# Optimization experiments

Hardware: AMD Instinct MI355X
Metric: run time of the kernel (lower is better)

Reference implementation:

```python
import jax, jax.numpy as jnp
import numpy as np

Bsz, L, D, N = 2, 2048, 1024, 16
LN_EPS = 1e-5


def setup_inputs() -> dict:
    key = jax.random.key(0)
    ks = jax.random.split(key, 5)
    # A_log initialized as in the module: -log(arange(1, N+1)) broadcast over D
    A_log = -jnp.broadcast_to(jnp.log(jnp.arange(1, N + 1, dtype=jnp.float32))[None, :], (D, N))
    return {
        "x": jax.random.normal(ks[0], (Bsz, L, D), jnp.float32),
        "W_dt": jax.random.normal(ks[1], (D, D), jnp.float32) * 0.02,
        "b_dt": jnp.zeros((D,), jnp.float32),
        "W_B": jax.random.normal(ks[2], (N, D), jnp.float32) * 0.02,
        "W_C": jax.random.normal(ks[3], (N, D), jnp.float32) * 0.02,
        "D_param": jnp.ones((D,), jnp.float32),
        "A_log": A_log,
        "gamma": jnp.ones((D,), jnp.float32),
        "beta": jnp.zeros((D,), jnp.float32),
    }


def reference(x, W_dt, b_dt, W_B, W_C, D_param, A_log, gamma, beta):
    residual = x
    # LayerNorm (biased variance, eps=1e-5)
    mu = jnp.mean(x, axis=-1, keepdims=True)
    var = jnp.var(x, axis=-1, keepdims=True)
    xn = (x - mu) * jax.lax.rsqrt(var + LN_EPS) * gamma + beta

    dt = jax.nn.softplus(xn @ W_dt.T + b_dt)          # (B, L, D)
    A = -jnp.exp(A_log)                                # (D, N)
    B_in = xn @ W_B.T                                  # (B, L, N)
    C_in = xn @ W_C.T                                  # (B, L, N)

    A_bar = jnp.exp(dt[..., None] * A)                 # (B, L, D, N)
    # B_bar[t] * x[t] fused: dt * B_in * xn -> (B, L, D, N)
    Bx = dt[..., None] * B_in[:, :, None, :] * xn[..., None]

    def step(h, inputs):
        a_t, bx_t, c_t = inputs                        # (B,D,N), (B,D,N), (B,N)
        h = a_t * h + bx_t                             # (B, D, N)
        y_t = jnp.einsum('bn,bdn->bd', c_t, h)         # (B, D)
        return h, y_t

    h0 = jnp.zeros((x.shape[0], D, N), x.dtype)
    _, ys = jax.lax.scan(
        step, h0,
        (jnp.transpose(A_bar, (1, 0, 2, 3)),
         jnp.transpose(Bx, (1, 0, 2, 3)),
         jnp.transpose(C_in, (1, 0, 2))))
    y = jnp.transpose(ys, (1, 0, 2)) + D_param * residual
    return y
```

## Files before the change

kernel.cpp:

```cpp
#include <hip/hip_runtime.h>
#include <hip/hip_cooperative_groups.h>
#include <cstddef>

namespace cg = cooperative_groups;

#define Bsz 2
#define Lr  2048
#define Dr  1024
#define Nr  16
#define M_ROWS (Bsz*Lr)
#define NPAD   1088
#define CHUNK  32
#define NCH    (Lr/CHUNK)

#define BM 64
#define BN 64
#define BK 64
#define NK (Dr/BK)

typedef __attribute__((ext_vector_type(8))) __bf16 bf16x8;
typedef __attribute__((ext_vector_type(4))) float floatx4;

__device__ __forceinline__ unsigned short f2bf(float f) {
    unsigned u = __float_as_uint(f);
    u += 0x7fffu + ((u >> 16) & 1u);
    return (unsigned short)(u >> 16);
}

__device__ __forceinline__ float bf2f(unsigned short u) {
    return __uint_as_float(((unsigned)u) << 16);
}

__device__ __forceinline__ float softplus_f(float x) {
    if (x > 0.f) return x + __logf(1.f + __expf(-x));
    return __logf(1.f + __expf(x));
}

__device__ __forceinline__ void gload_lds16(const unsigned short* g, unsigned short* l) {
    __builtin_amdgcn_global_load_lds((const __attribute__((address_space(1))) void*)g,
                                     (__attribute__((address_space(3))) void*)l, 16, 0, 0);
}

__global__ __launch_bounds__(256) void ln_pack_kernel(const float* __restrict__ x,
                                                      const float* __restrict__ gamma,
                                                      const float* __restrict__ beta,
                                                      unsigned short* __restrict__ xnb,
                                                      const float* __restrict__ Wdt,
                                                      const float* __restrict__ WB,
                                                      const float* __restrict__ WC,
                                                      unsigned short* __restrict__ Wcat) {
    if (blockIdx.x >= M_ROWS) {
        int i = (blockIdx.x - M_ROWS) * 256 + threadIdx.x;
        int row = i >> 10;
        int col = i & 1023;
        float v;
        if (row < Dr)                 v = Wdt[i];
        else if (row < Dr + Nr)       v = WB[(row - Dr) * Dr + col];
        else if (row < Dr + 2*Nr)     v = WC[(row - Dr - Nr) * Dr + col];
        else                          v = 0.f;
        Wcat[i] = f2bf(v);
        return;
    }
    int row = blockIdx.x;
    int tid = threadIdx.x;
    const float4* xr = (const float4*)(x + (size_t)row * Dr);
    float4 v = xr[tid];
    float s  = v.x + v.y + v.z + v.w;
    float ss = v.x*v.x + v.y*v.y + v.z*v.z + v.w*v.w;
    #pragma unroll
    for (int off = 32; off > 0; off >>= 1) {
        s  += __shfl_down(s, off);
        ss += __shfl_down(ss, off);
    }
    __shared__ float red[8];
    int wid = tid >> 6;
    if ((tid & 63) == 0) { red[wid*2] = s; red[wid*2+1] = ss; }
    __syncthreads();
    if (tid == 0) {
        float S = 0.f, SS = 0.f;
        #pragma unroll
        for (int w = 0; w < 4; w++) { S += red[w*2]; SS += red[w*2+1]; }
        float mu  = S * (1.f/Dr);
        float var = SS * (1.f/Dr) - mu*mu;
        red[0] = mu;
        red[1] = rsqrtf(var + 1e-5f);
    }
    __syncthreads();
    float mu = red[0], rs = red[1];
    float4 g = ((const float4*)gamma)[tid], bt = ((const float4*)beta)[tid];
    float4 o;
    o.x = (v.x - mu) * rs * g.x + bt.x;
    o.y = (v.y - mu) * rs * g.y + bt.y;
    o.z = (v.z - mu) * rs * g.z + bt.z;
    o.w = (v.w - mu) * rs * g.w + bt.w;
    ushort4 ob;
    ob.x = f2bf(o.x); ob.y = f2bf(o.y); ob.z = f2bf(o.z); ob.w = f2bf(o.w);
    ((ushort4*)(xnb + (size_t)row * Dr))[tid] = ob;
}

__global__ __launch_bounds__(256) void gemm_kernel(const unsigned short* __restrict__ xnb,
                                                   const unsigned short* __restrict__ w,
                                                   const float* __restrict__ b_dt,
                                                   unsigned short* __restrict__ dt,
                                                   float* __restrict__ bin,
                                                   float* __restrict__ cin) {
    __shared__ unsigned short As[BM * BK];
    __shared__ unsigned short Bs[BN * BK];
    int tid  = threadIdx.x;
    int wave = tid >> 6;
    int lane = tid & 63;
    int lm   = lane & 15;
    int quad = lane >> 4;
    int bid  = blockIdx.x;
    int xcd  = bid & 7;
    int j0   = bid >> 3;
    int nt   = j0 % 17;
    int mt   = (j0 / 17) * 8 + xcd;
    int Mb = mt * BM;
    int Nb = nt * BN;
    int wm = (wave >> 1) * 32;
    int wn = (wave & 1)  * 32;
    int koff = (mt + nt) & (NK - 1);

    int r0 = tid >> 3,        cg0 = (tid & 7) ^ (r0 & 7);
    int r1 = (tid + 256) >> 3, cg1 = ((tid + 256) & 7) ^ (r1 & 7);
    const unsigned short* Ag0 = xnb + (size_t)(Mb + r0) * Dr + cg0 * 8;
    const unsigned short* Ag1 = xnb + (size_t)(Mb + r1) * Dr + cg1 * 8;
    const unsigned short* Bg0 = w   + (size_t)(Nb + r0) * Dr + cg0 * 8;
    const unsigned short* Bg1 = w   + (size_t)(Nb + r1) * Dr + cg1 * 8;
    unsigned short* Al0 = &As[(size_t)tid * 8];
    unsigned short* Al1 = &As[(size_t)(tid + 256) * 8];
    unsigned short* Bl0 = &Bs[(size_t)tid * 8];
    unsigned short* Bl1 = &Bs[(size_t)(tid + 256) * 8];

    floatx4 acc[2][2] = {};

    for (int kk = 0; kk < NK; kk++) {
        int k0 = ((kk + koff) & (NK - 1)) * BK;
        gload_lds16(Ag0 + k0, Al0);
        gload_lds16(Ag1 + k0, Al1);
        gload_lds16(Bg0 + k0, Bl0);
        gload_lds16(Bg1 + k0, Bl1);
        __syncthreads();
        #pragma unroll
        for (int s = 0; s < 2; s++) {
            int ra0 = wm + lm, ra1 = wm + 16 + lm;
            int rb0 = wn + lm, rb1 = wn + 16 + lm;
            int cg = s * 4 + quad;
            bf16x8 a0 = *(const bf16x8*)&As[ra0 * BK + ((cg ^ (ra0 & 7)) * 8)];
            bf16x8 a1 = *(const bf16x8*)&As[ra1 * BK + ((cg ^ (ra1 & 7)) * 8)];
            bf16x8 b0 = *(const bf16x8*)&Bs[rb0 * BK + ((cg ^ (rb0 & 7)) * 8)];
            bf16x8 b1 = *(const bf16x8*)&Bs[rb1 * BK + ((cg ^ (rb1 & 7)) * 8)];
            acc[0][0] = __builtin_amdgcn_mfma_f32_16x16x32_bf16(a0, b0, acc[0][0], 0, 0, 0);
            acc[0][1] = __builtin_amdgcn_mfma_f32_16x16x32_bf16(a0, b1, acc[0][1], 0, 0, 0);
            acc[1][0] = __builtin_amdgcn_mfma_f32_16x16x32_bf16(a1, b0, acc[1][0], 0, 0, 0);
            acc[1][1] = __builtin_amdgcn_mfma_f32_16x16x32_bf16(a1, b1, acc[1][1], 0, 0, 0);
        }
        __syncthreads();
    }

    #pragma unroll
    for (int i = 0; i < 2; i++) {
        int grow0 = Mb + wm + i * 16 + quad * 4;
        #pragma unroll
        for (int jj = 0; jj < 2; jj++) {
            int gcol = Nb + wn + jj * 16 + lm;
            #pragma unroll
            for (int r = 0; r < 4; r++) {
                float v = acc[i][jj][r];
                int row = grow0 + r;
                if (gcol < Dr) {
                    dt[(size_t)row * Dr + gcol] = f2bf(softplus_f(v + b_dt[gcol]));
                } else if (gcol < Dr + Nr) {
                    bin[(size_t)row * Nr + (gcol - Dr)] = v;
                } else if (gcol < Dr + 2*Nr) {
                    cin[(size_t)row * Nr + (gcol - Dr - Nr)] = v;
                }
            }
        }
    }
}

__global__ __launch_bounds__(256, 2) void scan_fused_kernel(
        const unsigned short* __restrict__ dtb,
        const unsigned short* __restrict__ xnb,
        const float* __restrict__ bin,
        const float* __restrict__ cin,
        const float* __restrict__ A_log,
        const float* __restrict__ x,
        const float* __restrict__ Dp,
        float* __restrict__ Pws,
        float* __restrict__ hendws,
        float* __restrict__ hinws,
        float* __restrict__ out) {
    cg::grid_group grid = cg::this_grid();
    int tid  = threadIdx.x;
    int bid  = blockIdx.x;
    int dblk = bid & 3;
    int ch   = (bid >> 2) & 63;
    int b    = bid >> 8;
    int d    = dblk * 256 + tid;
    size_t rowbase = (size_t)b * Lr + ch * CHUNK;

    float ac[16];
    #pragma unroll
    for (int i = 0; i < 4; i++) {
        float4 t = ((const float4*)(A_log + (size_t)d * Nr))[i];
        ac[i*4+0] = -__expf(t.x);
        ac[i*4+1] = -__expf(t.y);
        ac[i*4+2] = -__expf(t.z);
        ac[i*4+3] = -__expf(t.w);
    }

    __shared__ float lb[CHUNK * Nr];
    __shared__ float lc[CHUNK * Nr];
    for (int i = tid; i < CHUNK * Nr; i += 256) {
        lb[i] = bin[rowbase * Nr + i];
        lc[i] = cin[rowbase * Nr + i];
    }
    __syncthreads();

    float dtv[CHUNK], xv[CHUNK];
    {
        const unsigned short* dtp = dtb + rowbase * Dr + d;
        const unsigned short* xp  = xnb + rowbase * Dr + d;
        #pragma unroll
        for (int t = 0; t < CHUNK; t++) {
            dtv[t] = bf2f(dtp[(size_t)t * Dr]);
            xv[t]  = bf2f(xp[(size_t)t * Dr]);
        }
    }

    float h[16];
    #pragma unroll
    for (int n = 0; n < 16; n++) h[n] = 0.f;
    float S = 0.f;
    #pragma unroll
    for (int t = 0; t < CHUNK; t++) {
        float dv = dtv[t];
        S += dv;
        float cm = dv * xv[t];
        const float4* br4 = (const float4*)(lb + t * Nr);
        float4 q0 = br4[0], q1 = br4[1], q2 = br4[2], q3 = br4[3];
        float bb[16] = {q0.x,q0.y,q0.z,q0.w, q1.x,q1.y,q1.z,q1.w,
                        q2.x,q2.y,q2.z,q2.w, q3.x,q3.y,q3.z,q3.w};
        #pragma unroll
        for (int n = 0; n < 16; n++)
            h[n] = __expf(dv * ac[n]) * h[n] + cm * bb[n];
    }
    size_t obase = ((size_t)(b * NCH + ch) * Nr) * Dr + d;
    #pragma unroll
    for (int n = 0; n < 16; n++) {
        Pws[obase + (size_t)n * Dr]    = __expf(S * ac[n]);
        hendws[obase + (size_t)n * Dr] = h[n];
    }

    grid.sync();

    if (bid < 128) {
        int id = bid * 256 + tid;
        int b2 = id >> 14;
        int dn = id & 16383;
        size_t base = ((size_t)b2 * NCH) * (Nr * Dr) + dn;
        float hin = 0.f;
        for (int cb = 0; cb < NCH; cb += 4) {
            float p[4], he[4];
            #pragma unroll
            for (int u = 0; u < 4; u++) {
                size_t idx = base + (size_t)(cb + u) * (Nr * Dr);
                p[u]  = Pws[idx];
                he[u] = hendws[idx];
            }
            #pragma unroll
            for (int u = 0; u < 4; u++) {
                size_t idx = base + (size_t)(cb + u) * (Nr * Dr);
                hinws[idx] = hin;
                hin = p[u] * hin + he[u];
            }
        }
    }

    grid.sync();

    #pragma unroll
    for (int n = 0; n < 16; n++) h[n] = hinws[obase + (size_t)n * Dr];
    float dp = Dp[d];
    const float* xr = x   + rowbase * Dr + d;
    float* op       = out + rowbase * Dr + d;

    for (int tb = 0; tb < CHUNK; tb += 4) {
        float xr4[4];
        #pragma unroll
        for (int u = 0; u < 4; u++) xr4[u] = xr[(size_t)(tb + u) * Dr];
        #pragma unroll
        for (int u = 0; u < 4; u++) {
            int t = tb + u;
            float dv = dtv[t];
            float cm = dv * xv[t];
            const float4* br4 = (const float4*)(lb + t * Nr);
            const float4* cr4 = (const float4*)(lc + t * Nr);
            float4 q0 = br4[0], q1 = br4[1], q2 = br4[2], q3 = br4[3];
            float4 r0 = cr4[0], r1 = cr4[1], r2 = cr4[2], r3 = cr4[3];
            float bb[16] = {q0.x,q0.y,q0.z,q0.w, q1.x,q1.y,q1.z,q1.w,
                            q2.x,q2.y,q2.z,q2.w, q3.x,q3.y,q3.z,q3.w};
            float cc[16] = {r0.x,r0.y,r0.z,r0.w, r1.x,r1.y,r1.z,r1.w,
                            r2.x,r2.y,r2.z,r2.w, r3.x,r3.y,r3.z,r3.w};
            float y = 0.f;
            #pragma unroll
            for (int n = 0; n < 16; n++) {
                h[n] = __expf(dv * ac[n]) * h[n] + cm * bb[n];
                y += cc[n] * h[n];
            }
            op[(size_t)t * Dr] = y + dp * xr4[u];
        }
    }
}

__global__ __launch_bounds__(256) void scan1_kernel(const unsigned short* __restrict__ dtb,
                                                    const unsigned short* __restrict__ xnb,
                                                    const float* __restrict__ bin,
                                                    const float* __restrict__ A_log,
                                                    float* __restrict__ Pws,
                                                    float* __restrict__ hendws) {
    int d  = blockIdx.x * 256 + threadIdx.x;
    int ch = blockIdx.y;
    int b  = blockIdx.z;
    size_t rowbase = (size_t)b * Lr + ch * CHUNK;

    float ac[16];
    #pragma unroll
    for (int i = 0; i < 4; i++) {
        float4 t = ((const float4*)(A_log + (size_t)d * Nr))[i];
        ac[i*4+0] = -__expf(t.x);
        ac[i*4+1] = -__expf(t.y);
        ac[i*4+2] = -__expf(t.z);
        ac[i*4+3] = -__expf(t.w);
    }

    __shared__ float lb[CHUNK * Nr];
    for (int i = threadIdx.x; i < CHUNK * Nr; i += 256)
        lb[i] = bin[rowbase * Nr + i];
    __syncthreads();

    float h[16];
    #pragma unroll
    for (int n = 0; n < 16; n++) h[n] = 0.f;
    float S = 0.f;

    const unsigned short* dtp = dtb + rowbase * Dr + d;
    const unsigned short* xp  = xnb + rowbase * Dr + d;

    for (int tb = 0; tb < CHUNK; tb += 4) {
        float dt4[4], xv4[4];
        #pragma unroll
        for (int u = 0; u < 4; u++) {
            dt4[u] = bf2f(dtp[(size_t)(tb + u) * Dr]);
            xv4[u] = bf2f(xp[(size_t)(tb + u) * Dr]);
        }
        #pragma unroll
        for (int u = 0; u < 4; u++) {
            float dv = dt4[u];
            S += dv;
            float cm = dv * xv4[u];
            const float4* br4 = (const float4*)(lb + (tb + u) * Nr);
            float4 q0 = br4[0], q1 = br4[1], q2 = br4[2], q3 = br4[3];
            float bb[16] = {q0.x,q0.y,q0.z,q0.w, q1.x,q1.y,q1.z,q1.w,
                            q2.x,q2.y,q2.z,q2.w, q3.x,q3.y,q3.z,q3.w};
            #pragma unroll
            for (int n = 0; n < 16; n++)
                h[n] = __expf(dv * ac[n]) * h[n] + cm * bb[n];
        }
    }

    size_t obase = ((size_t)(b * NCH + ch) * Nr) * Dr + d;
    #pragma unroll
    for (int n = 0; n < 16; n++) {
        Pws[obase + (size_t)n * Dr]    = __expf(S * ac[n]);
        hendws[obase + (size_t)n * Dr] = h[n];
    }
}

__global__ __launch_bounds__(256) void combine_kernel(const float* __restrict__ Pws,
                                                      const float* __restrict__ hendws,
                                                      float* __restrict__ hinws) {
    int id = blockIdx.x * 256 + threadIdx.x;
    int b  = id >> 14;
    int dn = id & 16383;
    size_t base = ((size_t)b * NCH) * (Nr * Dr) + dn;
    float hin = 0.f;
    for (int cb = 0; cb < NCH; cb += 4) {
        float p[4], he[4];
        #pragma unroll
        for (int u = 0; u < 4; u++) {
            size_t idx = base + (size_t)(cb + u) * (Nr * Dr);
            p[u]  = Pws[idx];
            he[u] = hendws[idx];
        }
        #pragma unroll
        for (int u = 0; u < 4; u++) {
            size_t idx = base + (size_t)(cb + u) * (Nr * Dr);
            hinws[idx] = hin;
            hin = p[u] * hin + he[u];
        }
    }
}

__global__ __launch_bounds__(256) void scan2_kernel(const unsigned short* __restrict__ dtb,
                                                    const unsigned short* __restrict__ xnb,
                                                    const float* __restrict__ bin,
                                                    const float* __restrict__ cin,
                                                    const float* __restrict__ A_log,
                                                    const float* __restrict__ hinws,
                                                    const float* __restrict__ x,
                                                    const float* __restrict__ Dp,
                                                    float* __restrict__ out) {
    int d  = blockIdx.x * 256 + threadIdx.x;
    int ch = blockIdx.y;
    int b  = blockIdx.z;
    size_t rowbase = (size_t)b * Lr + ch * CHUNK;

    float ac[16];
    #pragma unroll
    for (int i = 0; i < 4; i++) {
        float4 t = ((const float4*)(A_log + (size_t)d * Nr))[i];
        ac[i*4+0] = -__expf(t.x);
        ac[i*4+1] = -__expf(t.y);
        ac[i*4+2] = -__expf(t.z);
        ac[i*4+3] = -__expf(t.w);
    }

    __shared__ float lb[CHUNK * Nr];
    __shared__ float lc[CHUNK * Nr];
    for (int i = threadIdx.x; i < CHUNK * Nr; i += 256) {
        lb[i] = bin[rowbase * Nr + i];
        lc[i] = cin[rowbase * Nr + i];
    }
    __syncthreads();

    size_t obase = ((size_t)(b * NCH + ch) * Nr) * Dr + d;
    float h[16];
    #pragma unroll
    for (int n = 0; n < 16; n++) h[n] = hinws[obase + (size_t)n * Dr];

    float dp = Dp[d];
    const unsigned short* dtp = dtb + rowbase * Dr + d;
    const unsigned short* xp  = xnb + rowbase * Dr + d;
    const float* xr           = x   + rowbase * Dr + d;
    float* op                 = out + rowbase * Dr + d;

    for (int tb = 0; tb < CHUNK; tb += 4) {
        float dt4[4], xv4[4], xr4[4];
        #pragma unroll
        for (int u = 0; u < 4; u++) {
            dt4[u] = bf2f(dtp[(size_t)(tb + u) * Dr]);
            xv4[u] = bf2f(xp[(size_t)(tb + u) * Dr]);
            xr4[u] = xr[(size_t)(tb + u) * Dr];
        }
        #pragma unroll
        for (int u = 0; u < 4; u++) {
            float dv = dt4[u];
            float cm = dv * xv4[u];
            const float4* br4 = (const float4*)(lb + (tb + u) * Nr);
            const float4* cr4 = (const float4*)(lc + (tb + u) * Nr);
            float4 q0 = br4[0], q1 = br4[1], q2 = br4[2], q3 = br4[3];
            float4 r0 = cr4[0], r1 = cr4[1], r2 = cr4[2], r3 = cr4[3];
            float bb[16] = {q0.x,q0.y,q0.z,q0.w, q1.x,q1.y,q1.z,q1.w,
                            q2.x,q2.y,q2.z,q2.w, q3.x,q3.y,q3.z,q3.w};
            float cc[16] = {r0.x,r0.y,r0.z,r0.w, r1.x,r1.y,r1.z,r1.w,
                            r2.x,r2.y,r2.z,r2.w, r3.x,r3.y,r3.z,r3.w};
            float y = 0.f;
            #pragma unroll
            for (int n = 0; n < 16; n++) {
                h[n] = __expf(dv * ac[n]) * h[n] + cm * bb[n];
                y += cc[n] * h[n];
            }
            op[(size_t)(tb + u) * Dr] = y + dp * xr4[u];
        }
    }
}

extern "C" void kernel_launch(void* const* d_in, const int* in_sizes, int n_in,
                              void* d_out, int out_size, void* d_ws, size_t ws_size,
                              hipStream_t stream) {
    const float* x      = (const float*)d_in[0];
    const float* W_dt   = (const float*)d_in[1];
    const float* b_dt   = (const float*)d_in[2];
    const float* W_B    = (const float*)d_in[3];
    const float* W_C    = (const float*)d_in[4];
    const float* Dparam = (const float*)d_in[5];
    const float* A_log  = (const float*)d_in[6];
    const float* gamma  = (const float*)d_in[7];
    const float* beta   = (const float*)d_in[8];
    float* out = (float*)d_out;

    char* ws = (char*)d_ws;
    unsigned short* xnb  = (unsigned short*)(ws);
    unsigned short* wcat = (unsigned short*)(ws + 8388608);
    unsigned short* dtb  = (unsigned short*)(ws + 10616832);
    float*          bin  = (float*)(ws + 19005440);
    float*          cin  = (float*)(ws + 19267584);
    float*          Pws  = (float*)(ws + 19529728);
    float*          hend = (float*)(ws + 27918336);
    float*          hin  = (float*)(ws + 36306944);

    ln_pack_kernel<<<M_ROWS + (NPAD * Dr) / 256, 256, 0, stream>>>(
        x, gamma, beta, xnb, W_dt, W_B, W_C, wcat);
    gemm_kernel<<<(M_ROWS / BM) * (NPAD / BN), 256, 0, stream>>>(xnb, wcat, b_dt, dtb, bin, cin);

    int maxBlk = 0;
    hipError_t qerr = hipOccupancyMaxActiveBlocksPerMultiprocessor(
        &maxBlk, (const void*)scan_fused_kernel, 256, 0);
    bool coop_done = false;
    if (qerr == hipSuccess && maxBlk >= 2) {
        void* args[] = {
            (void*)&dtb, (void*)&xnb, (void*)&bin, (void*)&cin, (void*)&A_log,
            (void*)&x, (void*)&Dparam, (void*)&Pws, (void*)&hend, (void*)&hin, (void*)&out
        };
        hipError_t e = hipLaunchCooperativeKernel((const void*)scan_fused_kernel,
                                                  dim3(512), dim3(256),
                                                  args, 0, stream);
        coop_done = (e == hipSuccess);
    }
    if (!coop_done) {
        dim3 sgrid(Dr / 256, NCH, Bsz);
        scan1_kernel<<<sgrid, 256, 0, stream>>>(dtb, xnb, bin, A_log, Pws, hend);
        combine_kernel<<<(Bsz * Dr * Nr) / 256, 256, 0, stream>>>(Pws, hend, hin);
        scan2_kernel<<<sgrid, 256, 0, stream>>>(dtb, xnb, bin, cin, A_log, hin, x, Dparam, out);
    }
}
```

Before: 159.6 us.

## Replace cooperative fused scan with three-kernel chunked scan using bf16 carries

Drops the cooperative-launch fused scan, whose two grid-wide barriers required it to fit in 512 resident blocks, and goes back to separate scan1/combine/scan2 kernels. The chunk length is halved to 16 so the launch has more blocks and each thread has a shorter serial recurrence. Chunk decay products, chunk-end states and carried-in states are stored as bf16 to cut workspace traffic. In exchange there are twice as many chunks for the serial combine pass and bf16 rounding on the carried states, which may cost accuracy.

```diff
diff --git a/kernel.cpp b/kernel.cpp
--- a/kernel.cpp
+++ b/kernel.cpp
@@ -1,8 +1,5 @@
 #include <hip/hip_runtime.h>
-#include <hip/hip_cooperative_groups.h>
 #include <cstddef>
-
-namespace cg = cooperative_groups;
 
 #define Bsz 2
 #define Lr  2048
@@ -10,7 +7,7 @@
 #define Nr  16
 #define M_ROWS (Bsz*Lr)
 #define NPAD   1088
-#define CHUNK  32
+#define CHUNK  16
 #define NCH    (Lr/CHUNK)
 
 #define BM 64
@@ -122,7 +119,7 @@
     int wn = (wave & 1)  * 32;
     int koff = (mt + nt) & (NK - 1);
 
-    int r0 = tid >> 3,        cg0 = (tid & 7) ^ (r0 & 7);
+    int r0 = tid >> 3,         cg0 = (tid & 7) ^ (r0 & 7);
     int r1 = (tid + 256) >> 3, cg1 = ((tid + 256) & 7) ^ (r1 & 7);
     const unsigned short* Ag0 = xnb + (size_t)(Mb + r0) * Dr + cg0 * 8;
     const unsigned short* Ag1 = xnb + (size_t)(Mb + r1) * Dr + cg1 * 8;
@@ -181,25 +178,16 @@
     }
 }
 
-__global__ __launch_bounds__(256, 2) void scan_fused_kernel(
-        const unsigned short* __restrict__ dtb,
-        const unsigned short* __restrict__ xnb,
-        const float* __restrict__ bin,
-        const float* __restrict__ cin,
-        const float* __restrict__ A_log,
-        const float* __restrict__ x,
-        const float* __restrict__ Dp,
-        float* __restrict__ Pws,
-        float* __restrict__ hendws,
-        float* __restrict__ hinws,
-        float* __restrict__ out) {
-    cg::grid_group grid = cg::this_grid();
-    int tid  = threadIdx.x;
-    int bid  = blockIdx.x;
-    int dblk = bid & 3;
-    int ch   = (bid >> 2) & 63;
-    int b    = bid >> 8;
-    int d    = dblk * 256 + tid;
+__global__ __launch_bounds__(256) void scan1_kernel(const unsigned short* __restrict__ dtb,
+                                                    const unsigned short* __restrict__ xnb,
+                                                    const float* __restrict__ bin,
+                                                    const float* __restrict__ A_log,
+                                                    unsigned short* __restrict__ Pws,
+                                                    unsigned short* __restrict__ hendws) {
+    int tid = threadIdx.x;
+    int d  = blockIdx.x * 256 + tid;
+    int ch = blockIdx.y;
+    int b  = blockIdx.z;
     size_t rowbase = (size_t)b * Lr + ch * CHUNK;
 
     float ac[16];
@@ -213,11 +201,7 @@
     }
 
     __shared__ float lb[CHUNK * Nr];
-    __shared__ float lc[CHUNK * Nr];
-    for (int i = tid; i < CHUNK * Nr; i += 256) {
-        lb[i] = bin[rowbase * Nr + i];
-        lc[i] = cin[rowbase * Nr + i];
-    }
+    lb[tid] = bin[rowbase * Nr + tid];
     __syncthreads();
 
     float dtv[CHUNK], xv[CHUNK];
@@ -235,6 +219,7 @@
     #pragma unroll
     for (int n = 0; n < 16; n++) h[n] = 0.f;
     float S = 0.f;
+
     #pragma unroll
     for (int t = 0; t < CHUNK; t++) {
         float dv = dtv[t];
@@ -248,42 +233,87 @@
         for (int n = 0; n < 16; n++)
             h[n] = __expf(dv * ac[n]) * h[n] + cm * bb[n];
     }
+
     size_t obase = ((size_t)(b * NCH + ch) * Nr) * Dr + d;
     #pragma unroll
     for (int n = 0; n < 16; n++) {
-        Pws[obase + (size_t)n * Dr]    = __expf(S * ac[n]);
-        hendws[obase + (size_t)n * Dr] = h[n];
-    }
-
-    grid.sync();
-
-    if (bid < 128) {
-        int id = bid * 256 + tid;
-        int b2 = id >> 14;
-        int dn = id & 16383;
-        size_t base = ((size_t)b2 * NCH) * (Nr * Dr) + dn;
-        float hin = 0.f;
-        for (int cb = 0; cb < NCH; cb += 4) {
-            float p[4], he[4];
-            #pragma unroll
-            for (int u = 0; u < 4; u++) {
-                size_t idx = base + (size_t)(cb + u) * (Nr * Dr);
-                p[u]  = Pws[idx];
-                he[u] = hendws[idx];
-            }
-            #pragma unroll
-            for (int u = 0; u < 4; u++) {
-                size_t idx = base + (size_t)(cb + u) * (Nr * Dr);
-                hinws[idx] = hin;
-                hin = p[u] * hin + he[u];
-            }
-        }
-    }
-
-    grid.sync();
-
-    #pragma unroll
-    for (int n = 0; n < 16; n++) h[n] = hinws[obase + (size_t)n * Dr];
+        Pws[obase + (size_t)n * Dr]    = f2bf(__expf(S * ac[n]));
+        hendws[obase + (size_t)n * Dr] = f2bf(h[n]);
+    }
+}
+
+__global__ __launch_bounds__(256) void combine_kernel(const unsigned short* __restrict__ Pws,
+                                                      const unsigned short* __restrict__ hendws,
+                                                      unsigned short* __restrict__ hinws) {
+    int id = blockIdx.x * 256 + threadIdx.x;
+    int b  = id >> 14;
+    int dn = id & 16383;
+    size_t base = ((size_t)b * NCH) * (Nr * Dr) + dn;
+    float hin = 0.f;
+    for (int cb = 0; cb < NCH; cb += 8) {
+        float p[8], he[8];
+        #pragma unroll
+        for (int u = 0; u < 8; u++) {
+            size_t idx = base + (size_t)(cb + u) * (Nr * Dr);
+            p[u]  = bf2f(Pws[idx]);
+            he[u] = bf2f(hendws[idx]);
+        }
+        #pragma unroll
+        for (int u = 0; u < 8; u++) {
+            size_t idx = base + (size_t)(cb + u) * (Nr * Dr);
+            hinws[idx] = f2bf(hin);
+            hin = p[u] * hin + he[u];
+        }
+    }
+}
+
+__global__ __launch_bounds__(256) void scan2_kernel(const unsigned short* __restrict__ dtb,
+                                                    const unsigned short* __restrict__ xnb,
+                                                    const float* __restrict__ bin,
+                                                    const float* __restrict__ cin,
+                                                    const float* __restrict__ A_log,
+                                                    const unsigned short* __restrict__ hinws,
+                                                    const float* __restrict__ x,
+                                                    const float* __restrict__ Dp,
+                                                    float* __restrict__ out) {
+    int tid = threadIdx.x;
+    int d  = blockIdx.x * 256 + tid;
+    int ch = blockIdx.y;
+    int b  = blockIdx.z;
+    size_t rowbase = (size_t)b * Lr + ch * CHUNK;
+
+    float ac[16];
+    #pragma unroll
+    for (int i = 0; i < 4; i++) {
+        float4 t = ((const float4*)(A_log + (size_t)d * Nr))[i];
+        ac[i*4+0] = -__expf(t.x);
+        ac[i*4+1] = -__expf(t.y);
+        ac[i*4+2] = -__expf(t.z);
+        ac[i*4+3] = -__expf(t.w);
+    }
+
+    __shared__ float lb[CHUNK * Nr];
+    __shared__ float lc[CHUNK * Nr];
+    lb[tid] = bin[rowbase * Nr + tid];
+    lc[tid] = cin[rowbase * Nr + tid];
+    __syncthreads();
+
+    float dtv[CHUNK], xv[CHUNK];
+    {
+        const unsigned short* dtp = dtb + rowbase * Dr + d;
+        const unsigned short* xp  = xnb + rowbase * Dr + d;
+        #pragma unroll
+        for (int t = 0; t < CHUNK; t++) {
+            dtv[t] = bf2f(dtp[(size_t)t * Dr]);
+            xv[t]  = bf2f(xp[(size_t)t * Dr]);
+        }
+    }
+
+    size_t obase = ((size_t)(b * NCH + ch) * Nr) * Dr + d;
+    float h[16];
+    #pragma unroll
+    for (int n = 0; n < 16; n++) h[n] = bf2f(hinws[obase + (size_t)n * Dr]);
+
     float dp = Dp[d];
     const float* xr = x   + rowbase * Dr + d;
     float* op       = out + rowbase * Dr + d;
@@ -316,169 +346,6 @@
     }
 }
 
-__global__ __launch_bounds__(256) void scan1_kernel(const unsigned short* __restrict__ dtb,
-                                                    const unsigned short* __restrict__ xnb,
-                                                    const float* __restrict__ bin,
-                                                    const float* __restrict__ A_log,
-                                                    float* __restrict__ Pws,
-                                                    float* __restrict__ hendws) {
-    int d  = blockIdx.x * 256 + threadIdx.x;
-    int ch = blockIdx.y;
-    int b  = blockIdx.z;
-    size_t rowbase = (size_t)b * Lr + ch * CHUNK;
-
-    float ac[16];
-    #pragma unroll
-    for (int i = 0; i < 4; i++) {
-        float4 t = ((const float4*)(A_log + (size_t)d * Nr))[i];
-        ac[i*4+0] = -__expf(t.x);
-        ac[i*4+1] = -__expf(t.y);
-        ac[i*4+2] = -__expf(t.z);
-        ac[i*4+3] = -__expf(t.w);
-    }
-
-    __shared__ float lb[CHUNK * Nr];
-    for (int i = threadIdx.x; i < CHUNK * Nr; i += 256)
-        lb[i] = bin[rowbase * Nr + i];
-    __syncthreads();
-
-    float h[16];
-    #pragma unroll
-    for (int n = 0; n < 16; n++) h[n] = 0.f;
-    float S = 0.f;
-
-    const unsigned short* dtp = dtb + rowbase * Dr + d;
-    const unsigned short* xp  = xnb + rowbase * Dr + d;
-
-    for (int tb = 0; tb < CHUNK; tb += 4) {
-        float dt4[4], xv4[4];
-        #pragma unroll
-        for (int u = 0; u < 4; u++) {
-            dt4[u] = bf2f(dtp[(size_t)(tb + u) * Dr]);
-            xv4[u] = bf2f(xp[(size_t)(tb + u) * Dr]);
-        }
-        #pragma unroll
-        for (int u = 0; u < 4; u++) {
-            float dv = dt4[u];
-            S += dv;
-            float cm = dv * xv4[u];
-            const float4* br4 = (const float4*)(lb + (tb + u) * Nr);
-            float4 q0 = br4[0], q1 = br4[1], q2 = br4[2], q3 = br4[3];
-            float bb[16] = {q0.x,q0.y,q0.z,q0.w, q1.x,q1.y,q1.z,q1.w,
-                            q2.x,q2.y,q2.z,q2.w, q3.x,q3.y,q3.z,q3.w};
-            #pragma unroll
-            for (int n = 0; n < 16; n++)
-                h[n] = __expf(dv * ac[n]) * h[n] + cm * bb[n];
-        }
-    }
-
-    size_t obase = ((size_t)(b * NCH + ch) * Nr) * Dr + d;
-    #pragma unroll
-    for (int n = 0; n < 16; n++) {
-        Pws[obase + (size_t)n * Dr]    = __expf(S * ac[n]);
-        hendws[obase + (size_t)n * Dr] = h[n];
-    }
-}
-
-__global__ __launch_bounds__(256) void combine_kernel(const float* __restrict__ Pws,
-                                                      const float* __restrict__ hendws,
-                                                      float* __restrict__ hinws) {
-    int id = blockIdx.x * 256 + threadIdx.x;
-    int b  = id >> 14;
-    int dn = id & 16383;
-    size_t base = ((size_t)b * NCH) * (Nr * Dr) + dn;
-    float hin = 0.f;
-    for (int cb = 0; cb < NCH; cb += 4) {
-        float p[4], he[4];
-        #pragma unroll
-        for (int u = 0; u < 4; u++) {
-            size_t idx = base + (size_t)(cb + u) * (Nr * Dr);
-            p[u]  = Pws[idx];
-            he[u] = hendws[idx];
-        }
-        #pragma unroll
-        for (int u = 0; u < 4; u++) {
-            size_t idx = base + (size_t)(cb + u) * (Nr * Dr);
-            hinws[idx] = hin;
-            hin = p[u] * hin + he[u];
-        }
-    }
-}
-
-__global__ __launch_bounds__(256) void scan2_kernel(const unsigned short* __restrict__ dtb,
-                                                    const unsigned short* __restrict__ xnb,
-                                                    const float* __restrict__ bin,
-                                                    const float* __restrict__ cin,
-                                                    const float* __restrict__ A_log,
-                                                    const float* __restrict__ hinws,
-                                                    const float* __restrict__ x,
-                                                    const float* __restrict__ Dp,
-                                                    float* __restrict__ out) {
-    int d  = blockIdx.x * 256 + threadIdx.x;
-    int ch = blockIdx.y;
-    int b  = blockIdx.z;
-    size_t rowbase = (size_t)b * Lr + ch * CHUNK;
-
-    float ac[16];
-    #pragma unroll
-    for (int i = 0; i < 4; i++) {
-        float4 t = ((const float4*)(A_log + (size_t)d * Nr))[i];
-        ac[i*4+0] = -__expf(t.x);
-        ac[i*4+1] = -__expf(t.y);
-        ac[i*4+2] = -__expf(t.z);
-        ac[i*4+3] = -__expf(t.w);
-    }
-
-    __shared__ float lb[CHUNK * Nr];
-    __shared__ float lc[CHUNK * Nr];
-    for (int i = threadIdx.x; i < CHUNK * Nr; i += 256) {
-        lb[i] = bin[rowbase * Nr + i];
-        lc[i] = cin[rowbase * Nr + i];
-    }
-    __syncthreads();
-
-    size_t obase = ((size_t)(b * NCH + ch) * Nr) * Dr + d;
-    float h[16];
-    #pragma unroll
-    for (int n = 0; n < 16; n++) h[n] = hinws[obase + (size_t)n * Dr];
-
-    float dp = Dp[d];
-    const unsigned short* dtp = dtb + rowbase * Dr + d;
-    const unsigned short* xp  = xnb + rowbase * Dr + d;
-    const float* xr           = x   + rowbase * Dr + d;
-    float* op                 = out + rowbase * Dr + d;
-
-    for (int tb = 0; tb < CHUNK; tb += 4) {
-        float dt4[4], xv4[4], xr4[4];
-        #pragma unroll
-        for (int u = 0; u < 4; u++) {
-            dt4[u] = bf2f(dtp[(size_t)(tb + u) * Dr]);
-            xv4[u] = bf2f(xp[(size_t)(tb + u) * Dr]);
-            xr4[u] = xr[(size_t)(tb + u) * Dr];
-        }
-        #pragma unroll
-        for (int u = 0; u < 4; u++) {
-            float dv = dt4[u];
-            float cm = dv * xv4[u];
-            const float4* br4 = (const float4*)(lb + (tb + u) * Nr);
-            const float4* cr4 = (const float4*)(lc + (tb + u) * Nr);
-            float4 q0 = br4[0], q1 = br4[1], q2 = br4[2], q3 = br4[3];
-            float4 r0 = cr4[0], r1 = cr4[1], r2 = cr4[2], r3 = cr4[3];
-            float bb[16] = {q0.x,q0.y,q0.z,q0.w, q1.x,q1.y,q1.z,q1.w,
-                            q2.x,q2.y,q2.z,q2.w, q3.x,q3.y,q3.z,q3.w};
-            float cc[16] = {r0.x,r0.y,r0.z,r0.w, r1.x,r1.y,r1.z,r1.w,
-                            r2.x,r2.y,r2.z,r2.w, r3.x,r3.y,r3.z,r3.w};
-            float y = 0.f;
-            #pragma unroll
-            for (int n = 0; n < 16; n++) {
-                h[n] = __expf(dv * ac[n]) * h[n] + cm * bb[n];
-                y += cc[n] * h[n];
-            }
-            op[(size_t)(tb + u) * Dr] = y + dp * xr4[u];
-        }
-    }
-}
-
 extern "C" void kernel_launch(void* const* d_in, const int* in_sizes, int n_in,
                               void* d_out, int out_size, void* d_ws, size_t ws_size,
                               hipStream_t stream) {
@@ -499,32 +366,15 @@
     unsigned short* dtb  = (unsigned short*)(ws + 10616832);
     float*          bin  = (float*)(ws + 19005440);
     float*          cin  = (float*)(ws + 19267584);
-    float*          Pws  = (float*)(ws + 19529728);
-    float*          hend = (float*)(ws + 27918336);
-    float*          hin  = (float*)(ws + 36306944);
+    unsigned short* Pws  = (unsigned short*)(ws + 19529728);
+    unsigned short* hend = (unsigned short*)(ws + 27918336);
+    unsigned short* hin  = (unsigned short*)(ws + 36306944);
 
     ln_pack_kernel<<<M_ROWS + (NPAD * Dr) / 256, 256, 0, stream>>>(
         x, gamma, beta, xnb, W_dt, W_B, W_C, wcat);
     gemm_kernel<<<(M_ROWS / BM) * (NPAD / BN), 256, 0, stream>>>(xnb, wcat, b_dt, dtb, bin, cin);
-
-    int maxBlk = 0;
-    hipError_t qerr = hipOccupancyMaxActiveBlocksPerMultiprocessor(
-        &maxBlk, (const void*)scan_fused_kernel, 256, 0);
-    bool coop_done = false;
-    if (qerr == hipSuccess && maxBlk >= 2) {
-        void* args[] = {
-            (void*)&dtb, (void*)&xnb, (void*)&bin, (void*)&cin, (void*)&A_log,
-            (void*)&x, (void*)&Dparam, (void*)&Pws, (void*)&hend, (void*)&hin, (void*)&out
-        };
-        hipError_t e = hipLaunchCooperativeKernel((const void*)scan_fused_kernel,
-                                                  dim3(512), dim3(256),
-                                                  args, 0, stream);
-        coop_done = (e == hipSuccess);
-    }
-    if (!coop_done) {
-        dim3 sgrid(Dr / 256, NCH, Bsz);
-        scan1_kernel<<<sgrid, 256, 0, stream>>>(dtb, xnb, bin, A_log, Pws, hend);
-        combine_kernel<<<(Bsz * Dr * Nr) / 256, 256, 0, stream>>>(Pws, hend, hin);
-        scan2_kernel<<<sgrid, 256, 0, stream>>>(dtb, xnb, bin, cin, A_log, hin, x, Dparam, out);
-    }
-}
+    dim3 sgrid(Dr / 256, NCH, Bsz);
+    scan1_kernel<<<sgrid, 256, 0, stream>>>(dtb, xnb, bin, A_log, Pws, hend);
+    combine_kernel<<<(Bsz * Dr * Nr) / 256, 256, 0, stream>>>(Pws, hend, hin);
+    scan2_kernel<<<sgrid, 256, 0, stream>>>(dtb, xnb, bin, cin, A_log, hin, x, Dparam, out);
+}
```

After: 149.6 us. 6.3% less time.
